# Performance work log

Measured on AMD Instinct MI355X. Metric: run time of the kernel, lower is better.

The kernel has to match this reference:

```python
import jax, jax.numpy as jnp
import numpy as np

B, N, C = 16, 1025, 1024
H, D = 16, 64          # num_heads, head_dim
NPT = 1                # num_prefix_tokens
EPS = 1e-6
SCALE = D ** -0.5


def layer_norm(x, g, b, eps=EPS):
    mu = jnp.mean(x, axis=-1, keepdims=True)
    var = jnp.mean(jnp.square(x - mu), axis=-1, keepdims=True)
    return (x - mu) * jax.lax.rsqrt(var + eps) * g + b


def rot(x):
    # interleaved rotate-half: out[..., ::2] = -x[..., 1::2]; out[..., 1::2] = x[..., ::2]
    x2 = x.reshape(*x.shape[:-1], -1, 2)
    return jnp.stack([-x2[..., 1], x2[..., 0]], axis=-1).reshape(x.shape)


def apply_rot_embed_cat(x, emb):
    # emb: (N_spatial, 2*D) = [sin | cos]
    sin_emb, cos_emb = jnp.split(emb, 2, axis=-1)
    return x * cos_emb + rot(x) * sin_emb


def setup_inputs() -> dict:
    key = jax.random.key(0)
    ks = jax.random.split(key, 12)
    s = 0.02
    return {
        "x": jax.random.normal(ks[0], (B, N, C), jnp.float32),
        "rope": jax.random.normal(ks[1], (N - NPT, 2 * D), jnp.float32),
        "qkv_w": jax.random.normal(ks[2], (3 * C, C), jnp.float32) * s,
        "q_bias": jax.random.normal(ks[3], (C,), jnp.float32) * s,
        "k_bias": jnp.zeros((C,), jnp.float32),  # registered buffer, always zero
        "v_bias": jax.random.normal(ks[4], (C,), jnp.float32) * s,
        "qn_g": jnp.ones((D,), jnp.float32),
        "qn_b": jnp.zeros((D,), jnp.float32),
        "kn_g": jnp.ones((D,), jnp.float32),
        "kn_b": jnp.zeros((D,), jnp.float32),
        "norm_g": jnp.ones((C,), jnp.float32),
        "norm_b": jnp.zeros((C,), jnp.float32),
        "proj_w": jax.random.normal(ks[5], (C, C), jnp.float32) * s,
        "proj_b": jnp.zeros((C,), jnp.float32),
    }


def reference(x, rope, qkv_w, q_bias, k_bias, v_bias, qn_g, qn_b, kn_g, kn_b,
              norm_g, norm_b, proj_w, proj_b):
    b, n, c = x.shape
    qkv_bias = jnp.concatenate([q_bias, k_bias, v_bias])
    qkv = jnp.einsum('bnc,oc->bno', x, qkv_w) + qkv_bias          # (B,N,3C)
    qkv = qkv.reshape(b, n, 3, H, D).transpose(2, 0, 3, 1, 4)     # (3,B,H,N,D)
    q, k, v = qkv[0], qkv[1], qkv[2]
    # per-head QK layernorm over head_dim
    q = layer_norm(q, qn_g, qn_b)
    k = layer_norm(k, kn_g, kn_b)
    # RoPE on spatial tokens only (prefix tokens excluded)
    q = jnp.concatenate([q[:, :, :NPT], apply_rot_embed_cat(q[:, :, NPT:], rope)], axis=2)
    k = jnp.concatenate([k[:, :, :NPT], apply_rot_embed_cat(k[:, :, NPT:], rope)], axis=2)
    # scaled dot product attention
    attn = jnp.einsum('bhqd,bhkd->bhqk', q * SCALE, k)
    attn = jax.nn.softmax(attn, axis=-1)
    out = jnp.einsum('bhqk,bhkd->bhqd', attn, v)                  # (B,H,N,D)
    out = out.transpose(0, 2, 1, 3).reshape(b, n, c)              # (B,N,C)
    out = layer_norm(out, norm_g, norm_b)                         # scale_norm
    out = jnp.einsum('bnc,oc->bno', out, proj_w) + proj_b
    return out
```

## Files before the change

kernel.cpp:

```cpp
#include <hip/hip_runtime.h>
#include <hip/hip_bf16.h>

#define B_ 16
#define N_ 1025
#define C_ 1024
#define H_ 16
#define D_ 64
#define M_ (B_ * N_)
#define EPS_ 1e-6f
#define SCALE_ 0.125f
#define VTS_ 1088

typedef __attribute__((ext_vector_type(8))) short bf16x8;
typedef __attribute__((ext_vector_type(4))) float f32x4;
typedef unsigned short u16;
typedef unsigned int u32;

__device__ inline float bf2f(u16 h) {
    union { u32 u; float f; } c; c.u = ((u32)h) << 16; return c.f;
}
__device__ inline u16 f2bf(float f) {
    union { u32 u; float f; } c; c.f = f;
    u32 r = c.u + 0x7FFF + ((c.u >> 16) & 1);
    return (u16)(r >> 16);
}
__device__ inline u32 cvtpk(float lo, float hi) {
    u32 r;
    asm("v_cvt_pk_bf16_f32 %0, %1, %2" : "=v"(r) : "v"(lo), "v"(hi));
    return r;
}

__device__ inline void gload16(const void* g, void* l) {
    __builtin_amdgcn_global_load_lds(
        (const __attribute__((address_space(1))) void*)g,
        (__attribute__((address_space(3))) void*)l, 16, 0, 0);
}

__global__ void k_sniff(const u32* __restrict__ norm_g_bits, int* __restrict__ flag)
{
    if (threadIdx.x == 0 && blockIdx.x == 0)
        flag[0] = (norm_g_bits[0] == 0x3F800000u) ? 1 : 0;
}

__global__ __launch_bounds__(256) void k_convert(
    const void* __restrict__ src, u16* __restrict__ dst, long n,
    const int* __restrict__ flag)
{
    const int f = flag[0];
    long i0 = ((long)blockIdx.x * 256 + threadIdx.x) * 4;
    long stride = (long)gridDim.x * 1024;
    if (f) {
        const float* s = (const float*)src;
        for (long i = i0; i < n; i += stride) {
#pragma unroll
            for (int j = 0; j < 4; ++j) dst[i + j] = f2bf(s[i + j]);
        }
    } else {
        const u16* s = (const u16*)src;
        for (long i = i0; i < n; i += stride) {
#pragma unroll
            for (int j = 0; j < 4; ++j) dst[i + j] = s[i + j];
        }
    }
}

__global__ __launch_bounds__(256) void k_convert_small(
    const void* s0, const void* s1, const void* s2, const void* s3,
    const void* s4, const void* s5, const void* s6, const void* s7,
    const void* s8, const void* s9, u16* __restrict__ dst,
    const int* __restrict__ flag)
{
    int i = blockIdx.x * 256 + threadIdx.x;
    if (i >= 6400) return;
    const void* src; int off;
    if      (i < 1024) { src = s0; off = i; }
    else if (i < 2048) { src = s1; off = i - 1024; }
    else if (i < 3072) { src = s2; off = i - 2048; }
    else if (i < 3136) { src = s3; off = i - 3072; }
    else if (i < 3200) { src = s4; off = i - 3136; }
    else if (i < 3264) { src = s5; off = i - 3200; }
    else if (i < 3328) { src = s6; off = i - 3264; }
    else if (i < 4352) { src = s7; off = i - 3328; }
    else if (i < 5376) { src = s8; off = i - 4352; }
    else               { src = s9; off = i - 5376; }
    dst[i] = flag[0] ? f2bf(((const float*)src)[off]) : ((const u16*)src)[off];
}

__global__ __launch_bounds__(256) void k_qkv(
    const u16* __restrict__ x, const u16* __restrict__ wmat,
    const u16* __restrict__ qbias, const u16* __restrict__ kbias,
    const u16* __restrict__ vbias,
    u16* __restrict__ q, u16* __restrict__ kk, u16* __restrict__ vv)
{
    __shared__ __attribute__((aligned(16))) u16 As[128 * 32];
    __shared__ __attribute__((aligned(16))) u16 Bs[128 * 32];
    const int t  = threadIdx.x;
    const int m0 = blockIdx.y * 128;
    const int n0 = blockIdx.x * 128;
    const int w  = t >> 6;
    const int ln = t & 15;
    const int qd = (t & 63) >> 4;
    const int wr = (w >> 1) * 64;
    const int wc = (w & 1) * 64;

    f32x4 acc[4][4] = {};

    const int srow = t >> 2;
    const int scol = (t & 3) * 8;
    int ar0 = m0 + srow;       if (ar0 >= M_) ar0 = M_ - 1;
    int ar1 = m0 + 64 + srow;  if (ar1 >= M_) ar1 = M_ - 1;
    const u16* ap0 = x + (size_t)ar0 * C_ + scol;
    const u16* ap1 = x + (size_t)ar1 * C_ + scol;
    const u16* bp0 = wmat + (size_t)(n0 + srow) * C_ + scol;
    const u16* bp1 = wmat + (size_t)(n0 + 64 + srow) * C_ + scol;
    u16* lA0 = &As[t * 8];
    u16* lA1 = &As[2048 + t * 8];
    u16* lB0 = &Bs[t * 8];
    u16* lB1 = &Bs[2048 + t * 8];

    for (int k0 = 0; k0 < C_; k0 += 32) {
        gload16(ap0 + k0, lA0);
        gload16(ap1 + k0, lA1);
        gload16(bp0 + k0, lB0);
        gload16(bp1 + k0, lB1);
        __syncthreads();
        bf16x8 a[4], b[4];
#pragma unroll
        for (int i = 0; i < 4; ++i)
            a[i] = *(const bf16x8*)&As[(wr + i * 16 + ln) * 32 + qd * 8];
#pragma unroll
        for (int j = 0; j < 4; ++j)
            b[j] = *(const bf16x8*)&Bs[(wc + j * 16 + ln) * 32 + qd * 8];
#pragma unroll
        for (int i = 0; i < 4; ++i)
#pragma unroll
            for (int j = 0; j < 4; ++j)
                acc[i][j] = __builtin_amdgcn_mfma_f32_16x16x32_bf16(a[i], b[j], acc[i][j], 0, 0, 0);
        __syncthreads();
    }

#pragma unroll
    for (int j = 0; j < 4; ++j) {
        int o = n0 + wc + j * 16 + ln;
        int part = o >> 10;
        int c = o & 1023;
        int h = c >> 6, d = c & 63;
        const u16* bias = (part == 0) ? qbias : (part == 1) ? kbias : vbias;
        u16* dst = (part == 0) ? q : (part == 1) ? kk : vv;
        float bv = bf2f(bias[c]);
#pragma unroll
        for (int i = 0; i < 4; ++i) {
#pragma unroll
            for (int r = 0; r < 4; ++r) {
                int m = m0 + wr + i * 16 + qd * 4 + r;
                if (m >= M_) continue;
                int bb = m / N_, n = m % N_;
                dst[(((size_t)(bb * H_ + h)) * N_ + n) * D_ + d] = f2bf(acc[i][j][r] + bv);
            }
        }
    }
}

__global__ __launch_bounds__(256) void k_lnrope(
    u16* __restrict__ buf, const u16* __restrict__ g, const u16* __restrict__ bt,
    const u16* __restrict__ rope, float scale)
{
    int wid = (blockIdx.x * 256 + threadIdx.x) >> 6;
    int d = threadIdx.x & 63;
    if (wid >= B_ * H_ * N_) return;
    int n = wid % N_;
    u16* row = buf + (size_t)wid * 64;

    float xv = bf2f(row[d]);
    float s = xv;
#pragma unroll
    for (int off = 32; off; off >>= 1) s += __shfl_xor(s, off);
    float mu = s * (1.f / 64.f);
    float dv = xv - mu;
    float s2 = dv * dv;
#pragma unroll
    for (int off = 32; off; off >>= 1) s2 += __shfl_xor(s2, off);
    float var = s2 * (1.f / 64.f);
    float y = dv * rsqrtf(var + EPS_) * bf2f(g[d]) + bf2f(bt[d]);

    if (n >= 1) {
        const u16* rp = rope + (size_t)(n - 1) * 128;
        float sn = bf2f(rp[d]);
        float cs = bf2f(rp[64 + d]);
        float part = __shfl_xor(y, 1);
        float rot = (d & 1) ? part : -part;
        y = y * cs + rot * sn;
    }
    row[d] = f2bf(y * scale);
}

__global__ __launch_bounds__(256) void k_vt(
    const u16* __restrict__ v, u16* __restrict__ vt)
{
    const int kb = blockIdx.x % 17;
    const int bh = blockIdx.x / 17;
    const int k0 = kb * 64;
    const size_t src = (size_t)bh * N_ * D_;
    const size_t dst = (size_t)bh * D_ * VTS_;
    const int t = threadIdx.x;
    const int d = t & 63;
    const int kg0 = t >> 6;
#pragma unroll
    for (int c = 0; c < 2; ++c) {
        int kg = kg0 + c * 4;
        bf16x8 pk;
#pragma unroll
        for (int i = 0; i < 8; ++i) {
            int gk = k0 + kg * 8 + i; if (gk > N_ - 1) gk = N_ - 1;
            pk[i] = (short)v[src + (size_t)gk * D_ + d];
        }
        *(bf16x8*)(vt + dst + (size_t)d * VTS_ + k0 + kg * 8) = pk;
    }
}

__global__ __launch_bounds__(256) void k_attn(
    const u16* __restrict__ q, const u16* __restrict__ k,
    const u16* __restrict__ vt, u16* __restrict__ out)
{
    __shared__ __attribute__((aligned(16))) u16 Ks[64 * 72];
    __shared__ __attribute__((aligned(16))) u16 Vs[64 * 72];
    __shared__ __attribute__((aligned(16))) u16 Pt[4][16 * 72];

    const int t  = threadIdx.x;
    const int w  = t >> 6;
    const int ln = t & 15;
    const int qd = (t & 63) >> 4;

    const int qb = blockIdx.x % 9;
    const int bh = blockIdx.x / 9;
    const int b = bh >> 4, h = bh & 15;
    const size_t kbase = (size_t)bh * N_ * D_;
    const size_t vbase = (size_t)bh * D_ * VTS_;
    const int qw = qb * 128 + w * 32;

    bf16x8 qa[2][2];
#pragma unroll
    for (int a = 0; a < 2; ++a) {
        int row = qw + a * 16 + ln; if (row > N_ - 1) row = N_ - 1;
        const u16* qp = q + kbase + (size_t)row * D_;
        qa[a][0] = *(const bf16x8*)(qp + qd * 8);
        qa[a][1] = *(const bf16x8*)(qp + 32 + qd * 8);
    }

    f32x4 o_acc[2][4] = {};
    float m_run[2] = { -1e30f, -1e30f };
    float l_run[2] = { 0.f, 0.f };

    const int skey = t >> 3;
    const int sdg  = t & 7;

    bf16x8 pk[2], pv[2];
#pragma unroll
    for (int c = 0; c < 2; ++c) {
        int r32 = c * 32 + skey;
        pk[c] = *(const bf16x8*)(k + kbase + (size_t)r32 * D_ + sdg * 8);
        pv[c] = *(const bf16x8*)(vt + vbase + (size_t)r32 * VTS_ + sdg * 8);
    }

    for (int k0 = 0; k0 < N_; k0 += 64) {
#pragma unroll
        for (int c = 0; c < 2; ++c) {
            int r32 = c * 32 + skey;
            *(bf16x8*)&Ks[r32 * 72 + sdg * 8] = pk[c];
            *(bf16x8*)&Vs[r32 * 72 + sdg * 8] = pv[c];
        }
        __syncthreads();

        const int k1 = k0 + 64;
        if (k1 < N_) {
#pragma unroll
            for (int c = 0; c < 2; ++c) {
                int r32 = c * 32 + skey;
                int gk = k1 + r32; if (gk > N_ - 1) gk = N_ - 1;
                pk[c] = *(const bf16x8*)(k + kbase + (size_t)gk * D_ + sdg * 8);
                pv[c] = *(const bf16x8*)(vt + vbase + (size_t)r32 * VTS_ + k1 + sdg * 8);
            }
        }

        bf16x8 kf[4][2];
#pragma unroll
        for (int ks = 0; ks < 4; ++ks) {
            kf[ks][0] = *(const bf16x8*)&Ks[(ks * 16 + ln) * 72 + qd * 8];
            kf[ks][1] = *(const bf16x8*)&Ks[(ks * 16 + ln) * 72 + 32 + qd * 8];
        }

        bf16x8 pf[2][2];
        float alpha[2];
#pragma unroll
        for (int a = 0; a < 2; ++a) {
            f32x4 s[4] = {};
#pragma unroll
            for (int ks = 0; ks < 4; ++ks) {
                s[ks] = __builtin_amdgcn_mfma_f32_16x16x32_bf16(kf[ks][0], qa[a][0], s[ks], 0, 0, 0);
                s[ks] = __builtin_amdgcn_mfma_f32_16x16x32_bf16(kf[ks][1], qa[a][1], s[ks], 0, 0, 0);
            }
            if (k0 + 64 > N_) {
#pragma unroll
                for (int ks = 0; ks < 4; ++ks)
#pragma unroll
                    for (int r = 0; r < 4; ++r)
                        if (k0 + 16 * ks + 4 * qd + r > N_ - 1) s[ks][r] = -1e30f;
            }
            float t0 = fmaxf(fmaxf(s[0][0], s[0][1]), fmaxf(s[0][2], s[0][3]));
            float t1 = fmaxf(fmaxf(s[1][0], s[1][1]), fmaxf(s[1][2], s[1][3]));
            float t2 = fmaxf(fmaxf(s[2][0], s[2][1]), fmaxf(s[2][2], s[2][3]));
            float t3 = fmaxf(fmaxf(s[3][0], s[3][1]), fmaxf(s[3][2], s[3][3]));
            float mx = fmaxf(fmaxf(t0, t1), fmaxf(t2, t3));
            mx = fmaxf(mx, __shfl_xor(mx, 16));
            mx = fmaxf(mx, __shfl_xor(mx, 32));
            float mn = fmaxf(m_run[a], mx);
            alpha[a] = __expf(m_run[a] - mn);
            m_run[a] = mn;
            float rs = 0.f;
#pragma unroll
            for (int ks = 0; ks < 4; ++ks)
#pragma unroll
                for (int r = 0; r < 4; ++r) {
                    s[ks][r] = __expf(s[ks][r] - mn);
                    rs += s[ks][r];
                }
            rs += __shfl_xor(rs, 16);
            rs += __shfl_xor(rs, 32);
            l_run[a] = l_run[a] * alpha[a] + rs;

            u16* pt = &Pt[w][0];
#pragma unroll
            for (int ks = 0; ks < 4; ++ks) {
                *(u32*)&pt[ln * 72 + 16 * ks + 4 * qd]     = cvtpk(s[ks][0], s[ks][1]);
                *(u32*)&pt[ln * 72 + 16 * ks + 4 * qd + 2] = cvtpk(s[ks][2], s[ks][3]);
            }
            pf[a][0] = *(const bf16x8*)&pt[ln * 72 + qd * 8];
            pf[a][1] = *(const bf16x8*)&pt[ln * 72 + 32 + qd * 8];

#pragma unroll
            for (int nt = 0; nt < 4; ++nt)
#pragma unroll
                for (int r = 0; r < 4; ++r)
                    o_acc[a][nt][r] *= alpha[a];
        }

#pragma unroll
        for (int nt = 0; nt < 4; ++nt) {
            bf16x8 v0 = *(const bf16x8*)&Vs[(nt * 16 + ln) * 72 + qd * 8];
            bf16x8 v1 = *(const bf16x8*)&Vs[(nt * 16 + ln) * 72 + 32 + qd * 8];
#pragma unroll
            for (int a = 0; a < 2; ++a) {
                o_acc[a][nt] = __builtin_amdgcn_mfma_f32_16x16x32_bf16(v0, pf[a][0], o_acc[a][nt], 0, 0, 0);
                o_acc[a][nt] = __builtin_amdgcn_mfma_f32_16x16x32_bf16(v1, pf[a][1], o_acc[a][nt], 0, 0, 0);
            }
        }
        __syncthreads();
    }

#pragma unroll
    for (int a = 0; a < 2; ++a) {
        int n = qw + a * 16 + ln;
        if (n >= N_) continue;
        float lr = l_run[a];
        u16* op = out + ((size_t)b * N_ + n) * C_ + h * 64;
#pragma unroll
        for (int nt = 0; nt < 4; ++nt)
#pragma unroll
            for (int rp = 0; rp < 2; ++rp) {
                int d = nt * 16 + qd * 4 + rp * 2;
                *(u32*)&op[d] = cvtpk(o_acc[a][nt][rp * 2] / lr,
                                      o_acc[a][nt][rp * 2 + 1] / lr);
            }
    }
}

__global__ __launch_bounds__(256) void k_ln(
    const u16* __restrict__ in, const u16* __restrict__ g,
    const u16* __restrict__ bt, u16* __restrict__ outb)
{
    __shared__ float red[8];
    const int row = blockIdx.x;
    const int t = threadIdx.x;
    const u16* p = in + (size_t)row * C_;

    float vals[4];
    float s = 0.f;
#pragma unroll
    for (int i = 0; i < 4; ++i) { vals[i] = bf2f(p[t + i * 256]); s += vals[i]; }
#pragma unroll
    for (int off = 32; off; off >>= 1) s += __shfl_xor(s, off);
    if ((t & 63) == 0) red[t >> 6] = s;
    __syncthreads();
    float mu = (red[0] + red[1] + red[2] + red[3]) * (1.f / 1024.f);
    float s2 = 0.f;
#pragma unroll
    for (int i = 0; i < 4; ++i) { float d = vals[i] - mu; s2 += d * d; }
#pragma unroll
    for (int off = 32; off; off >>= 1) s2 += __shfl_xor(s2, off);
    __syncthreads();
    if ((t & 63) == 0) red[t >> 6] = s2;
    __syncthreads();
    float var = (red[0] + red[1] + red[2] + red[3]) * (1.f / 1024.f);
    float rs = rsqrtf(var + EPS_);
#pragma unroll
    for (int i = 0; i < 4; ++i) {
        int cidx = t + i * 256;
        float y = (vals[i] - mu) * rs * bf2f(g[cidx]) + bf2f(bt[cidx]);
        outb[(size_t)row * C_ + cidx] = f2bf(y);
    }
}

__global__ __launch_bounds__(256) void k_proj(
    const u16* __restrict__ y, const u16* __restrict__ wmat,
    const u16* __restrict__ bias, void* __restrict__ out,
    const int* __restrict__ flag)
{
    __shared__ __attribute__((aligned(16))) u16 As[128 * 32];
    __shared__ __attribute__((aligned(16))) u16 Bs[128 * 32];
    const int t  = threadIdx.x;
    const int m0 = blockIdx.y * 128;
    const int n0 = blockIdx.x * 128;
    const int w  = t >> 6;
    const int ln = t & 15;
    const int qd = (t & 63) >> 4;
    const int wr = (w >> 1) * 64;
    const int wc = (w & 1) * 64;

    f32x4 acc[4][4] = {};

    const int srow = t >> 2;
    const int scol = (t & 3) * 8;
    int ar0 = m0 + srow;       if (ar0 >= M_) ar0 = M_ - 1;
    int ar1 = m0 + 64 + srow;  if (ar1 >= M_) ar1 = M_ - 1;
    const u16* ap0 = y + (size_t)ar0 * C_ + scol;
    const u16* ap1 = y + (size_t)ar1 * C_ + scol;
    const u16* bp0 = wmat + (size_t)(n0 + srow) * C_ + scol;
    const u16* bp1 = wmat + (size_t)(n0 + 64 + srow) * C_ + scol;
    u16* lA0 = &As[t * 8];
    u16* lA1 = &As[2048 + t * 8];
    u16* lB0 = &Bs[t * 8];
    u16* lB1 = &Bs[2048 + t * 8];

    for (int k0 = 0; k0 < C_; k0 += 32) {
        gload16(ap0 + k0, lA0);
        gload16(ap1 + k0, lA1);
        gload16(bp0 + k0, lB0);
        gload16(bp1 + k0, lB1);
        __syncthreads();
        bf16x8 a[4], b[4];
#pragma unroll
        for (int i = 0; i < 4; ++i)
            a[i] = *(const bf16x8*)&As[(wr + i * 16 + ln) * 32 + qd * 8];
#pragma unroll
        for (int j = 0; j < 4; ++j)
            b[j] = *(const bf16x8*)&Bs[(wc + j * 16 + ln) * 32 + qd * 8];
#pragma unroll
        for (int i = 0; i < 4; ++i)
#pragma unroll
            for (int j = 0; j < 4; ++j)
                acc[i][j] = __builtin_amdgcn_mfma_f32_16x16x32_bf16(a[i], b[j], acc[i][j], 0, 0, 0);
        __syncthreads();
    }

    const int f32out = flag[0];
#pragma unroll
    for (int j = 0; j < 4; ++j) {
        int o = n0 + wc + j * 16 + ln;
        float bv = bf2f(bias[o]);
#pragma unroll
        for (int i = 0; i < 4; ++i) {
#pragma unroll
            for (int r = 0; r < 4; ++r) {
                int m = m0 + wr + i * 16 + qd * 4 + r;
                if (m >= M_) continue;
                float val = acc[i][j][r] + bv;
                if (f32out) ((float*)out)[(size_t)m * C_ + o] = val;
                else        ((u16*)out)[(size_t)m * C_ + o] = f2bf(val);
            }
        }
    }
}

extern "C" void kernel_launch(void* const* d_in, const int* in_sizes, int n_in,
                              void* d_out, int out_size, void* d_ws, size_t ws_size,
                              hipStream_t stream)
{
    char* ws = (char*)d_ws;
    int* flag = (int*)ws;
    u16* arena = (u16*)(ws + 256);

    const long X_OFF = 0,            X_N = (long)M_ * C_;
    const long R_OFF = X_OFF + X_N,  R_N = (long)(N_ - 1) * 2 * D_;
    const long W_OFF = R_OFF + R_N,  W_N = (long)3 * C_ * C_;
    const long P_OFF = W_OFF + W_N,  P_N = (long)C_ * C_;
    const long S_OFF = P_OFF + P_N;
    const long ARENA_N = S_OFF + 6400;

    u16* xb   = arena + X_OFF;
    u16* ropb = arena + R_OFF;
    u16* qkvw = arena + W_OFF;
    u16* pw   = arena + P_OFF;
    u16* qb   = arena + S_OFF;
    u16* kb   = qb + 1024;
    u16* vb   = kb + 1024;
    u16* qng  = vb + 1024;
    u16* qnb  = qng + 64;
    u16* kng  = qnb + 64;
    u16* knb  = kng + 64;
    u16* ng   = knb + 64;
    u16* nb   = ng + 1024;
    u16* pb   = nb + 1024;

    char* after = (char*)(arena + ARENA_N);
    const size_t sz = (size_t)B_ * H_ * N_ * D_ * 2;
    u16* qbuf = (u16*)after;
    u16* kbuf = (u16*)(after + sz);
    u16* vbuf = (u16*)(after + 2 * sz);
    u16* vtb  = (u16*)(after + 3 * sz);
    u16* ao   = xb;
    u16* ybuf = qbuf;

    k_sniff<<<1, 64, 0, stream>>>((const u32*)d_in[10], flag);

    k_convert<<<4096, 256, 0, stream>>>(d_in[0], xb, X_N, flag);
    k_convert<<<128, 256, 0, stream>>>(d_in[1], ropb, R_N, flag);
    k_convert<<<2048, 256, 0, stream>>>(d_in[2], qkvw, W_N, flag);
    k_convert<<<1024, 256, 0, stream>>>(d_in[12], pw, P_N, flag);
    k_convert_small<<<25, 256, 0, stream>>>(
        d_in[3], d_in[4], d_in[5], d_in[6], d_in[7], d_in[8], d_in[9],
        d_in[10], d_in[11], d_in[13], qb, flag);

    dim3 g1(24, 129);
    k_qkv<<<g1, 256, 0, stream>>>(xb, qkvw, qb, kb, vb, qbuf, kbuf, vbuf);

    const int rows = B_ * H_ * N_;
    k_lnrope<<<(rows + 3) / 4, 256, 0, stream>>>(qbuf, qng, qnb, ropb, SCALE_);
    k_lnrope<<<(rows + 3) / 4, 256, 0, stream>>>(kbuf, kng, knb, ropb, 1.0f);

    k_vt<<<B_ * H_ * 17, 256, 0, stream>>>(vbuf, vtb);

    k_attn<<<B_ * H_ * 9, 256, 0, stream>>>(qbuf, kbuf, vtb, ao);

    k_ln<<<M_, 256, 0, stream>>>(ao, ng, nb, ybuf);

    dim3 g2(8, 129);
    k_proj<<<g2, 256, 0, stream>>>(ybuf, pw, pb, d_out, flag);
}
```

Before: 664.0 us.

## Batch QK MFMAs across row tiles, skip unchanged-max rescale, add setprio

Issues all QK^T MFMAs for both 16-row query tiles back to back before any softmax work, and gives each tile its own P staging buffer so both tiles can be written before the PV reads. The online-softmax rescale of the accumulators is skipped when no lane's row max grew (a wave-uniform __any test). The MFMA regions are wrapped in s_setprio to favour matrix issue across waves. The intent is more independent MFMA work in flight and fewer VALU multiplies, at the cost of more live registers and twice the LDS for P.

```diff
diff --git a/kernel.cpp b/kernel.cpp
--- a/kernel.cpp
+++ b/kernel.cpp
@@ -224,7 +224,7 @@
 {
     __shared__ __attribute__((aligned(16))) u16 Ks[64 * 72];
     __shared__ __attribute__((aligned(16))) u16 Vs[64 * 72];
-    __shared__ __attribute__((aligned(16))) u16 Pt[4][16 * 72];
+    __shared__ __attribute__((aligned(16))) u16 Pt[4][2][16 * 72];
 
     const int t  = threadIdx.x;
     const int w  = t >> 6;
@@ -289,61 +289,83 @@
             kf[ks][1] = *(const bf16x8*)&Ks[(ks * 16 + ln) * 72 + 32 + qd * 8];
         }
 
-        bf16x8 pf[2][2];
-        float alpha[2];
+        f32x4 s2[2][4] = {};
+        __builtin_amdgcn_s_setprio(1);
+#pragma unroll
+        for (int a = 0; a < 2; ++a)
+#pragma unroll
+            for (int ks = 0; ks < 4; ++ks) {
+                s2[a][ks] = __builtin_amdgcn_mfma_f32_16x16x32_bf16(kf[ks][0], qa[a][0], s2[a][ks], 0, 0, 0);
+                s2[a][ks] = __builtin_amdgcn_mfma_f32_16x16x32_bf16(kf[ks][1], qa[a][1], s2[a][ks], 0, 0, 0);
+            }
+        __builtin_amdgcn_s_setprio(0);
+
+        if (k0 + 64 > N_) {
+#pragma unroll
+            for (int a = 0; a < 2; ++a)
+#pragma unroll
+                for (int ks = 0; ks < 4; ++ks)
+#pragma unroll
+                    for (int r = 0; r < 4; ++r)
+                        if (k0 + 16 * ks + 4 * qd + r > N_ - 1) s2[a][ks][r] = -1e30f;
+        }
+
+        float mx[2];
 #pragma unroll
         for (int a = 0; a < 2; ++a) {
-            f32x4 s[4] = {};
-#pragma unroll
-            for (int ks = 0; ks < 4; ++ks) {
-                s[ks] = __builtin_amdgcn_mfma_f32_16x16x32_bf16(kf[ks][0], qa[a][0], s[ks], 0, 0, 0);
-                s[ks] = __builtin_amdgcn_mfma_f32_16x16x32_bf16(kf[ks][1], qa[a][1], s[ks], 0, 0, 0);
-            }
-            if (k0 + 64 > N_) {
-#pragma unroll
-                for (int ks = 0; ks < 4; ++ks)
+            float t0 = fmaxf(fmaxf(s2[a][0][0], s2[a][0][1]), fmaxf(s2[a][0][2], s2[a][0][3]));
+            float t1 = fmaxf(fmaxf(s2[a][1][0], s2[a][1][1]), fmaxf(s2[a][1][2], s2[a][1][3]));
+            float t2 = fmaxf(fmaxf(s2[a][2][0], s2[a][2][1]), fmaxf(s2[a][2][2], s2[a][2][3]));
+            float t3 = fmaxf(fmaxf(s2[a][3][0], s2[a][3][1]), fmaxf(s2[a][3][2], s2[a][3][3]));
+            float m = fmaxf(fmaxf(t0, t1), fmaxf(t2, t3));
+            m = fmaxf(m, __shfl_xor(m, 16));
+            m = fmaxf(m, __shfl_xor(m, 32));
+            mx[a] = m;
+        }
+
+#pragma unroll
+        for (int a = 0; a < 2; ++a) {
+            if (__any(mx[a] > m_run[a])) {
+                float mn = fmaxf(m_run[a], mx[a]);
+                float al = __expf(m_run[a] - mn);
+                m_run[a] = mn;
+                l_run[a] *= al;
+#pragma unroll
+                for (int nt = 0; nt < 4; ++nt)
 #pragma unroll
                     for (int r = 0; r < 4; ++r)
-                        if (k0 + 16 * ks + 4 * qd + r > N_ - 1) s[ks][r] = -1e30f;
-            }
-            float t0 = fmaxf(fmaxf(s[0][0], s[0][1]), fmaxf(s[0][2], s[0][3]));
-            float t1 = fmaxf(fmaxf(s[1][0], s[1][1]), fmaxf(s[1][2], s[1][3]));
-            float t2 = fmaxf(fmaxf(s[2][0], s[2][1]), fmaxf(s[2][2], s[2][3]));
-            float t3 = fmaxf(fmaxf(s[3][0], s[3][1]), fmaxf(s[3][2], s[3][3]));
-            float mx = fmaxf(fmaxf(t0, t1), fmaxf(t2, t3));
-            mx = fmaxf(mx, __shfl_xor(mx, 16));
-            mx = fmaxf(mx, __shfl_xor(mx, 32));
-            float mn = fmaxf(m_run[a], mx);
-            alpha[a] = __expf(m_run[a] - mn);
-            m_run[a] = mn;
+                        o_acc[a][nt][r] *= al;
+            }
+            const float mcur = m_run[a];
             float rs = 0.f;
 #pragma unroll
             for (int ks = 0; ks < 4; ++ks)
 #pragma unroll
                 for (int r = 0; r < 4; ++r) {
-                    s[ks][r] = __expf(s[ks][r] - mn);
-                    rs += s[ks][r];
+                    s2[a][ks][r] = __expf(s2[a][ks][r] - mcur);
+                    rs += s2[a][ks][r];
                 }
             rs += __shfl_xor(rs, 16);
             rs += __shfl_xor(rs, 32);
-            l_run[a] = l_run[a] * alpha[a] + rs;
-
-            u16* pt = &Pt[w][0];
+            l_run[a] += rs;
+
+            u16* pt = &Pt[w][a][0];
 #pragma unroll
             for (int ks = 0; ks < 4; ++ks) {
-                *(u32*)&pt[ln * 72 + 16 * ks + 4 * qd]     = cvtpk(s[ks][0], s[ks][1]);
-                *(u32*)&pt[ln * 72 + 16 * ks + 4 * qd + 2] = cvtpk(s[ks][2], s[ks][3]);
-            }
+                *(u32*)&pt[ln * 72 + 16 * ks + 4 * qd]     = cvtpk(s2[a][ks][0], s2[a][ks][1]);
+                *(u32*)&pt[ln * 72 + 16 * ks + 4 * qd + 2] = cvtpk(s2[a][ks][2], s2[a][ks][3]);
+            }
+        }
+
+        bf16x8 pf[2][2];
+#pragma unroll
+        for (int a = 0; a < 2; ++a) {
+            const u16* pt = &Pt[w][a][0];
             pf[a][0] = *(const bf16x8*)&pt[ln * 72 + qd * 8];
             pf[a][1] = *(const bf16x8*)&pt[ln * 72 + 32 + qd * 8];
-
-#pragma unroll
-            for (int nt = 0; nt < 4; ++nt)
-#pragma unroll
-                for (int r = 0; r < 4; ++r)
-                    o_acc[a][nt][r] *= alpha[a];
-        }
-
+        }
+
+        __builtin_amdgcn_s_setprio(1);
 #pragma unroll
         for (int nt = 0; nt < 4; ++nt) {
             bf16x8 v0 = *(const bf16x8*)&Vs[(nt * 16 + ln) * 72 + qd * 8];
@@ -354,6 +376,7 @@
                 o_acc[a][nt] = __builtin_amdgcn_mfma_f32_16x16x32_bf16(v1, pf[a][1], o_acc[a][nt], 0, 0, 0);
             }
         }
+        __builtin_amdgcn_s_setprio(0);
         __syncthreads();
     }
 
```

New measurement: 665.7 us. No clear change (+0.3%).
